# Kernel tuning notes

Hardware: AMD Instinct MI355X
Metric: run time of the kernel (lower is better)

The kernel has to match this reference:

```python
import jax, jax.numpy as jnp
import numpy as np

HEADS, DIM_HEAD, DIM = 12, 64, 768
H = W = 32
N = H * W
B = 4


def _ln(x, g, b, eps=1e-5):
    mu = x.mean(-1, keepdims=True)
    var = ((x - mu) ** 2).mean(-1, keepdims=True)
    return (x - mu) / jnp.sqrt(var + eps) * g + b


def _get_epipolar(k, src_c2w, target_c2w, h=H, w=W):
    # Faithful port of Epipolar_Attention.get_epipolar, without the (hw*hw,3) repeat
    # materialization (uses broadcasting for the pairwise cross product instead).
    b = k.shape[0]
    Wf = h * 16.0 / 9.0
    k = k.astype(jnp.float32)
    k = k.at[:, 0, :].multiply(Wf).at[:, 1, :].multiply(float(h))
    k = k.at[:, 0, 2].set(h / 2.0).at[:, 1, 2].set(h / 2.0)
    ii, jj = jnp.meshgrid(jnp.arange(h), jnp.arange(w), indexing='ij')
    # after the torch column swap: (col, row, 1)
    coords = jnp.stack([jj.ravel(), ii.ravel(), jnp.ones(h * w, jnp.int32)], axis=1).astype(jnp.float32)  # [hw,3]
    k3 = k[:, :3, :3]
    src_r, src_t = src_c2w[:, :3, :3].astype(jnp.float32), src_c2w[:, :3, 3].astype(jnp.float32)
    tgt_r, tgt_t = target_c2w[:, :3, :3].astype(jnp.float32), target_c2w[:, :3, 3].astype(jnp.float32)
    tgt_rinv = jnp.linalg.inv(tgt_r)
    fx, fy = k3[:, 0, 0][:, None], k3[:, 1, 1][:, None]
    cx, cy = k3[:, 0, 2][:, None], k3[:, 1, 2][:, None]
    nc = jnp.stack([(coords[None, :, 0] - cx) / fx,
                    (coords[None, :, 1] - cy) / fy,
                    jnp.broadcast_to(coords[None, :, 2], (b, h * w))], axis=-1)  # [b,hw,3]
    p3w = jnp.einsum('bij,bnj->bni', src_r, nc) + src_t[:, None]
    p2 = jnp.einsum('bij,bnj->bni', tgt_rinv, p3w) - tgt_t[:, None]  # target_w2c_t = -target_c2w_t
    pij_un = jnp.einsum('bij,bnj->bni', k3, p2)                      # [b,hw,3]
    pij = pij_un / (pij_un[..., -1:] + 1e-6)
    o2 = jnp.einsum('bij,bj->bi', tgt_rinv, src_t) - tgt_t           # origin projected
    oij = jnp.einsum('bij,bj->bi', k3, o2)
    oij = oij / oij[..., -1:]
    oi_to_pi = pij - oij[:, None]                # [b,hw,3]
    oi_to_coord = coords[None] - oij[:, None]    # [b,hw,3]
    cr = jnp.cross(oi_to_pi[:, :, None, :], oi_to_coord[:, None, :, :])  # [b,hw,hw,3]
    area = jnp.sqrt((cr * cr).sum(-1))
    vlen = jnp.sqrt((oi_to_pi * oi_to_pi).sum(-1))[:, :, None]
    dist = area / vlen
    dw = 1.0 - jax.nn.sigmoid(50.0 * (dist - 0.5))
    row_max = dw.max(-1, keepdims=True)
    return jnp.where(row_max < 0.5, 1.0, dw)     # rows with max<0.5 are set to all-ones


def setup_inputs():
    key = jax.random.key(0)
    ks = jax.random.split(key, 16)
    s = 0.02
    x = jax.random.normal(ks[0], (B, N, DIM), jnp.float32)
    src_encode = jax.random.normal(ks[1], (B, N, DIM), jnp.float32)
    intrinsic = (jnp.zeros((B, 4, 4), jnp.float32)
                 .at[:, 0, 0].set(1.0).at[:, 1, 1].set(1.0)
                 .at[:, 0, 2].set(0.5).at[:, 1, 2].set(0.5)
                 .at[:, 2, 2].set(1.0).at[:, 3, 3].set(1.0))
    R = jnp.eye(3, dtype=jnp.float32) + 0.1 * jax.random.normal(ks[2], (2, B, 3, 3), jnp.float32)
    t = 0.5 * jax.random.normal(ks[3], (2, B, 3), jnp.float32)
    c2w = (jnp.zeros((2, B, 4, 4), jnp.float32)
           .at[:, :, :3, :3].set(R).at[:, :, :3, 3].set(t).at[:, :, 3, 3].set(1.0))
    hd = HEADS * DIM_HEAD
    w_ = lambda k_, shp: s * jax.random.normal(k_, shp, jnp.float32)
    return dict(
        x=x, src_encode=src_encode, intrinsic=intrinsic, c2w=c2w,
        lnq_g=jnp.ones(DIM), lnq_b=jnp.zeros(DIM), Wq=w_(ks[4], (DIM, hd)), bq=jnp.zeros(hd),
        lnk_g=jnp.ones(DIM), lnk_b=jnp.zeros(DIM), Wk=w_(ks[5], (DIM, hd)), bk=jnp.zeros(hd),
        lnv_g=jnp.ones(DIM), lnv_b=jnp.zeros(DIM), Wv=w_(ks[6], (DIM, hd)), bv=jnp.zeros(hd),
        Wp=w_(ks[7], (hd, DIM)), bp=jnp.zeros(DIM),
        pre_g=jnp.ones(DIM), pre_b=jnp.zeros(DIM),
        W1=w_(ks[8], (DIM, 2 * DIM)), b1=jnp.zeros(2 * DIM),
        W2=w_(ks[9], (2 * DIM, DIM)), b2=jnp.zeros(DIM),
        post_g=jnp.ones(DIM), post_b=jnp.zeros(DIM))


def reference(x, src_encode, intrinsic, c2w, lnq_g, lnq_b, Wq, bq, lnk_g, lnk_b, Wk, bk,
              lnv_g, lnv_b, Wv, bv, Wp, bp, pre_g, pre_b, W1, b1, W2, b2, post_g, post_b):
    b, n, _ = x.shape
    scale = DIM_HEAD ** -0.5
    split = lambda t_: t_.reshape(b, n, HEADS, DIM_HEAD).transpose(0, 2, 1, 3)  # [b,m,n,d]
    q = split(_ln(x, lnq_g, lnq_b) @ Wq + bq)
    k = split(_ln(src_encode, lnk_g, lnk_b) @ Wk + bk)
    v = split(_ln(src_encode, lnv_g, lnv_b) @ Wv + bv)
    scores = scale * jnp.einsum('bmqd,bmkd->bmqk', q, k)
    e1 = _get_epipolar(intrinsic, c2w[1], c2w[0])                    # do_epipolar
    e2 = jnp.swapaxes(_get_epipolar(intrinsic, c2w[0], c2w[1]), 1, 2)  # bidirectional (transposed)
    wmap = e1 * e2                                                   # [b,n,n], shared across heads
    att = jax.nn.softmax(scores * wmap[:, None], axis=-1)
    a = jnp.einsum('bmqk,bmkd->bmqd', att, v).transpose(0, 2, 1, 3).reshape(b, n, HEADS * DIM_HEAD)
    z = _ln(a @ Wp + bp, pre_g, pre_b)
    z = z + (jax.nn.gelu(z @ W1 + b1, approximate=False) @ W2 + b2)  # torch nn.GELU = exact erf
    z = _ln(z, post_g, post_b)
    wm_full = jnp.broadcast_to(wmap[:, None], (b, HEADS, n, n)).reshape(b * HEADS, n, n)
    return z, wm_full
```

## Files before the change

### kernel.cpp

```cpp
#include <hip/hip_runtime.h>
#include <hip/hip_bf16.h>

typedef unsigned short u16;
typedef __attribute__((ext_vector_type(4))) unsigned short u16x4;
typedef __attribute__((ext_vector_type(8))) unsigned short u16x8;
typedef __attribute__((ext_vector_type(8))) short s16x8;
typedef __attribute__((ext_vector_type(4))) float f32x4;

#define HEADS 12
#define NSEQ 1024
#define DIMM 768
#define DHEAD 64

__device__ __forceinline__ float b2f(u16 h) {
  union { unsigned u; float f; } v; v.u = ((unsigned)h) << 16; return v.f;
}
__device__ __forceinline__ u16 f2b(float f) {
  union { float f; unsigned u; } v; v.f = f;
  unsigned r = v.u + 0x7fffu + ((v.u >> 16) & 1u);
  return (u16)(r >> 16);
}
__device__ __forceinline__ void gl_lds16(const u16* g, u16* l) {
  __builtin_amdgcn_global_load_lds(
      (const __attribute__((address_space(1))) void*)g,
      (__attribute__((address_space(3))) void*)l, 16, 0, 0);
}

template<bool GELU, bool RESID>
__device__ __forceinline__ void gemm_body(
    const u16* __restrict__ A, const u16* __restrict__ BT,
    const float* __restrict__ bias, const u16* __restrict__ resid,
    const float* __restrict__ rg, const float* __restrict__ rb,
    u16* __restrict__ C, int K, int lda, int ldb, int ldc,
    int m0, int n0, u16* As, u16* Bs)
{
  const int tid = threadIdx.x;
  const int lane = tid & 63;
  const int wv = tid >> 6;
  const int wm0 = (wv >> 1) * 64;
  const int wn0 = (wv & 1) * 64;
  const int l15 = lane & 15;
  const int quad = lane >> 4;
  const int srow = lane >> 2;
  const int scol = (lane & 3) * 8;

  f32x4 acc[4][4];
  #pragma unroll
  for (int i = 0; i < 4; ++i)
    #pragma unroll
    for (int j = 0; j < 4; ++j)
      acc[i][j] = {0.f, 0.f, 0.f, 0.f};

  const u16* Ab = A + (long)(m0 + wv * 32 + srow) * lda + scol;
  const u16* Bb = BT + (long)(n0 + wv * 32 + srow) * ldb + scol;
  u16* AsW = As + (wv * 32) * 32;
  u16* BsW = Bs + (wv * 32) * 32;

  auto issue = [&](int buf, int kk) {
    #pragma unroll
    for (int t = 0; t < 2; ++t) {
      gl_lds16(Ab + kk + (long)t * 16 * lda, AsW + buf * 4096 + t * 16 * 32);
      gl_lds16(Bb + kk + (long)t * 16 * ldb, BsW + buf * 4096 + t * 16 * 32);
    }
  };

  const int NK = K >> 5;
  issue(0, 0);
  issue(1, 32);

  int cur = 0;
  for (int i = 0; i < NK; ++i) {
    if (i + 1 < NK) asm volatile("s_waitcnt vmcnt(4)" ::: "memory");
    else            asm volatile("s_waitcnt vmcnt(0)" ::: "memory");
    __builtin_amdgcn_s_barrier();
    __builtin_amdgcn_sched_barrier(0);
    if (i + 2 < NK) {
      int nb = cur + 2; if (nb >= 3) nb -= 3;
      issue(nb, (i + 2) * 32);
    }
    const u16* Ac = As + cur * 4096;
    const u16* Bc = Bs + cur * 4096;
    s16x8 af[4], bfr[4];
    #pragma unroll
    for (int i2 = 0; i2 < 4; ++i2)
      af[i2] = *(const s16x8*)&Ac[(wm0 + i2 * 16 + l15) * 32 + quad * 8];
    #pragma unroll
    for (int j = 0; j < 4; ++j)
      bfr[j] = *(const s16x8*)&Bc[(wn0 + j * 16 + l15) * 32 + quad * 8];
    #pragma unroll
    for (int i2 = 0; i2 < 4; ++i2)
      #pragma unroll
      for (int j = 0; j < 4; ++j)
        acc[i2][j] = __builtin_amdgcn_mfma_f32_16x16x32_bf16(af[i2], bfr[j], acc[i2][j], 0, 0, 0);
    ++cur; if (cur == 3) cur = 0;
  }

  #pragma unroll
  for (int i = 0; i < 4; ++i)
    #pragma unroll
    for (int j = 0; j < 4; ++j) {
      const int col = n0 + wn0 + j * 16 + l15;
      const float bvv = bias[col];
      #pragma unroll
      for (int v = 0; v < 4; ++v) {
        const int row = m0 + wm0 + i * 16 + quad * 4 + v;
        float val = acc[i][j][v] + bvv;
        if (GELU) val = 0.5f * val * (1.0f + erff(val * 0.70710678118654752440f));
        if (RESID) val += b2f(resid[(long)row * ldc + col]) * rg[col] + rb[col];
        C[(long)row * ldc + col] = f2b(val);
      }
    }
}

template<bool GELU, bool RESID>
__device__ __forceinline__ void gemm_body64(
    const u16* __restrict__ A, const u16* __restrict__ BT,
    const float* __restrict__ bias, const u16* __restrict__ resid,
    const float* __restrict__ rg, const float* __restrict__ rb,
    u16* __restrict__ C, int K, int lda, int ldb, int ldc,
    int m0, int n0, u16* As, u16* Bs)
{
  const int tid = threadIdx.x;
  const int lane = tid & 63;
  const int wv = tid >> 6;
  const int wm0 = wv * 32;
  const int l15 = lane & 15;
  const int quad = lane >> 4;
  const int srow = lane >> 2;
  const int scol = (lane & 3) * 8;

  f32x4 acc[2][4];
  #pragma unroll
  for (int i = 0; i < 2; ++i)
    #pragma unroll
    for (int j = 0; j < 4; ++j)
      acc[i][j] = {0.f, 0.f, 0.f, 0.f};

  const u16* Ab = A + (long)(m0 + wv * 32 + srow) * lda + scol;
  const u16* Bb = BT + (long)(n0 + wv * 16 + srow) * ldb + scol;
  u16* AsW = As + (wv * 32) * 32;
  u16* BsW = Bs + (wv * 16) * 32;

  auto issue = [&](int buf, int kk) {
    #pragma unroll
    for (int t = 0; t < 2; ++t)
      gl_lds16(Ab + kk + (long)t * 16 * lda, AsW + buf * 4096 + t * 16 * 32);
    gl_lds16(Bb + kk, BsW + buf * 2048);
  };

  const int NK = K >> 5;
  issue(0, 0);
  issue(1, 32);

  int cur = 0;
  for (int i = 0; i < NK; ++i) {
    if (i + 1 < NK) asm volatile("s_waitcnt vmcnt(3)" ::: "memory");
    else            asm volatile("s_waitcnt vmcnt(0)" ::: "memory");
    __builtin_amdgcn_s_barrier();
    __builtin_amdgcn_sched_barrier(0);
    if (i + 2 < NK) {
      int nb = cur + 2; if (nb >= 3) nb -= 3;
      issue(nb, (i + 2) * 32);
    }
    const u16* Ac = As + cur * 4096;
    const u16* Bc = Bs + cur * 2048;
    s16x8 af[2], bfr[4];
    #pragma unroll
    for (int i2 = 0; i2 < 2; ++i2)
      af[i2] = *(const s16x8*)&Ac[(wm0 + i2 * 16 + l15) * 32 + quad * 8];
    #pragma unroll
    for (int j = 0; j < 4; ++j)
      bfr[j] = *(const s16x8*)&Bc[(j * 16 + l15) * 32 + quad * 8];
    #pragma unroll
    for (int i2 = 0; i2 < 2; ++i2)
      #pragma unroll
      for (int j = 0; j < 4; ++j)
        acc[i2][j] = __builtin_amdgcn_mfma_f32_16x16x32_bf16(af[i2], bfr[j], acc[i2][j], 0, 0, 0);
    ++cur; if (cur == 3) cur = 0;
  }

  #pragma unroll
  for (int i = 0; i < 2; ++i)
    #pragma unroll
    for (int j = 0; j < 4; ++j) {
      const int col = n0 + j * 16 + l15;
      const float bvv = bias[col];
      #pragma unroll
      for (int v = 0; v < 4; ++v) {
        const int row = m0 + wm0 + i * 16 + quad * 4 + v;
        float val = acc[i][j][v] + bvv;
        if (GELU) val = 0.5f * val * (1.0f + erff(val * 0.70710678118654752440f));
        if (RESID) val += b2f(resid[(long)row * ldc + col]) * rg[col] + rb[col];
        C[(long)row * ldc + col] = f2b(val);
      }
    }
}

template<bool GELU, bool RESID>
__global__ __launch_bounds__(256)
void gemm_one(const u16* __restrict__ A, const u16* __restrict__ BT,
              const float* __restrict__ bias, const u16* __restrict__ resid,
              const float* __restrict__ rg, const float* __restrict__ rb,
              u16* __restrict__ C, int K, int lda, int ldb, int ldc)
{
  __shared__ u16 As[12288], Bs[6144];
  gemm_body64<GELU, RESID>(A, BT, bias, resid, rg, rb, C, K, lda, ldb, ldc,
                           blockIdx.x * 128, blockIdx.y * 64, As, Bs);
}

__global__ __launch_bounds__(256)
void gemm_qkv(const u16* __restrict__ nx, const u16* __restrict__ ns,
              const u16* __restrict__ qT, const u16* __restrict__ kvT,
              const float* __restrict__ bqf, const float* __restrict__ bkvf,
              u16* __restrict__ qb, u16* __restrict__ kvb)
{
  __shared__ u16 As[12288], Bs[12288];
  const int z = blockIdx.z;
  if (z == 0)
    gemm_body<false, false>(nx, qT, bqf, nullptr, nullptr, nullptr, qb,
                            768, 768, 768, 768,
                            blockIdx.x * 128, blockIdx.y * 128, As, Bs);
  else
    gemm_body<false, false>(ns, kvT, bkvf, nullptr, nullptr, nullptr, kvb,
                            768, 768, 768, 1536,
                            blockIdx.x * 128, (z - 1) * 768 + blockIdx.y * 128, As, Bs);
}

__global__ __launch_bounds__(256, 3)
void fattn(const u16* __restrict__ qb, const u16* __restrict__ kvb,
           const u16* __restrict__ vT, const u16* __restrict__ wm,
           u16* __restrict__ outA)
{
  __shared__ u16 Qs[2 * 64 * 32];
  __shared__ u16 Ks[2][2 * 64 * 32];
  __shared__ u16 Vs[2][2 * 64 * 32];
  __shared__ u16 Ps[64][72];

  const int bh = blockIdx.y;
  const int b = bh / HEADS, h = bh - b * HEADS;
  const int q0 = blockIdx.x * 64;
  const int tid = threadIdx.x;
  const int lane = tid & 63;
  const int wv = tid >> 6;
  const int l15 = lane & 15;
  const int quad = lane >> 4;
  const int srow = lane >> 2;
  const int scol = (lane & 3) * 8;

  const u16* Qg = qb + ((long)b * NSEQ + q0) * DIMM + h * DHEAD;
  const u16* Kg = kvb + (long)b * NSEQ * 1536 + h * DHEAD;
  const u16* Vg = vT + (long)bh * DHEAD * NSEQ;
  const u16* Wg = wm + ((long)b * NSEQ + q0) * NSEQ;

  #pragma unroll
  for (int h2 = 0; h2 < 2; ++h2) {
    gl_lds16(Qg + (long)(wv * 16 + srow) * DIMM + h2 * 32 + scol,
             Qs + (h2 * 64 + wv * 16) * 32);
    gl_lds16(Kg + (long)(wv * 16 + srow) * 1536 + h2 * 32 + scol,
             Ks[0] + (h2 * 64 + wv * 16) * 32);
    gl_lds16(Vg + (long)(wv * 16 + srow) * NSEQ + h2 * 32 + scol,
             Vs[0] + (h2 * 64 + wv * 16) * 32);
  }

  f32x4 Sacc[4], Oacc[4];
  float mrow[4], lrow[4];
  #pragma unroll
  for (int j = 0; j < 4; ++j) {
    Oacc[j] = {0.f, 0.f, 0.f, 0.f};
    mrow[j] = -3.0e38f;
    lrow[j] = 0.f;
  }
  s16x8 qf[2];

  int cur = 0;
  for (int kt = 0; kt < 16; ++kt) {
    __syncthreads();
    if (kt < 15) {
      const int nxt = cur ^ 1;
      #pragma unroll
      for (int h2 = 0; h2 < 2; ++h2) {
        gl_lds16(Kg + (long)((kt + 1) * 64 + wv * 16 + srow) * 1536 + h2 * 32 + scol,
                 Ks[nxt] + (h2 * 64 + wv * 16) * 32);
        gl_lds16(Vg + (long)(wv * 16 + srow) * NSEQ + (kt + 1) * 64 + h2 * 32 + scol,
                 Vs[nxt] + (h2 * 64 + wv * 16) * 32);
      }
    }

    if (kt == 0) {
      qf[0] = *(const s16x8*)&Qs[(0 * 64 + wv * 16 + l15) * 32 + quad * 8];
      qf[1] = *(const s16x8*)&Qs[(1 * 64 + wv * 16 + l15) * 32 + quad * 8];
    }

    float wr[4][4];
    #pragma unroll
    for (int j = 0; j < 4; ++j)
      #pragma unroll
      for (int v = 0; v < 4; ++v)
        wr[j][v] = b2f(Wg[(long)(wv * 16 + quad * 4 + v) * NSEQ + kt * 64 + j * 16 + l15]);

    #pragma unroll
    for (int j = 0; j < 4; ++j) Sacc[j] = {0.f, 0.f, 0.f, 0.f};
    #pragma unroll
    for (int j = 0; j < 4; ++j)
      #pragma unroll
      for (int h2 = 0; h2 < 2; ++h2) {
        s16x8 kf = *(const s16x8*)&Ks[cur][(h2 * 64 + j * 16 + l15) * 32 + quad * 8];
        Sacc[j] = __builtin_amdgcn_mfma_f32_16x16x32_bf16(qf[h2], kf, Sacc[j], 0, 0, 0);
      }

    #pragma unroll
    for (int j = 0; j < 4; ++j)
      #pragma unroll
      for (int v = 0; v < 4; ++v)
        Sacc[j][v] *= wr[j][v];
    #pragma unroll
    for (int v = 0; v < 4; ++v) {
      float tm = fmaxf(fmaxf(Sacc[0][v], Sacc[1][v]), fmaxf(Sacc[2][v], Sacc[3][v]));
      tm = fmaxf(tm, __shfl_xor(tm, 1));
      tm = fmaxf(tm, __shfl_xor(tm, 2));
      tm = fmaxf(tm, __shfl_xor(tm, 4));
      tm = fmaxf(tm, __shfl_xor(tm, 8));
      const float mnew = fmaxf(mrow[v], tm);
      const float al = __expf(mrow[v] - mnew);
      float rs = 0.f;
      #pragma unroll
      for (int j = 0; j < 4; ++j) {
        const float e = __expf(Sacc[j][v] - mnew);
        Sacc[j][v] = e;
        rs += e;
      }
      rs += __shfl_xor(rs, 1);
      rs += __shfl_xor(rs, 2);
      rs += __shfl_xor(rs, 4);
      rs += __shfl_xor(rs, 8);
      lrow[v] = lrow[v] * al + rs;
      mrow[v] = mnew;
      #pragma unroll
      for (int jn = 0; jn < 4; ++jn) Oacc[jn][v] *= al;
    }
    #pragma unroll
    for (int j = 0; j < 4; ++j)
      #pragma unroll
      for (int v = 0; v < 4; ++v)
        Ps[wv * 16 + quad * 4 + v][j * 16 + l15] = f2b(Sacc[j][v]);

    #pragma unroll
    for (int h2 = 0; h2 < 2; ++h2) {
      s16x8 af = *(const s16x8*)&Ps[wv * 16 + l15][h2 * 32 + quad * 8];
      #pragma unroll
      for (int jn = 0; jn < 4; ++jn) {
        s16x8 vf = *(const s16x8*)&Vs[cur][(h2 * 64 + jn * 16 + l15) * 32 + quad * 8];
        Oacc[jn] = __builtin_amdgcn_mfma_f32_16x16x32_bf16(af, vf, Oacc[jn], 0, 0, 0);
      }
    }
    cur ^= 1;
  }

  #pragma unroll
  for (int v = 0; v < 4; ++v) {
    const int row = q0 + wv * 16 + quad * 4 + v;
    const float inv = 1.0f / lrow[v];
    #pragma unroll
    for (int jn = 0; jn < 4; ++jn)
      outA[((long)(b * NSEQ + row)) * DIMM + h * DHEAD + jn * 16 + l15] =
          f2b(Oacc[jn][v] * inv);
  }
}

template<bool F32IN>
__global__ __launch_bounds__(256)
void norm_k(const void* __restrict__ in, u16* __restrict__ out)
{
  const long base = (long)blockIdx.x * DIMM;
  const int tid = threadIdx.x;
  __shared__ float s1[8], s2[8];
  float v0, v1, v2;
  if (F32IN) {
    const float* p = (const float*)in + base;
    v0 = p[tid]; v1 = p[tid + 256]; v2 = p[tid + 512];
  } else {
    const u16* p = (const u16*)in + base;
    v0 = b2f(p[tid]); v1 = b2f(p[tid + 256]); v2 = b2f(p[tid + 512]);
  }
  float s = v0 + v1 + v2;
  #pragma unroll
  for (int off = 32; off; off >>= 1) s += __shfl_down(s, off);
  const int lane = tid & 63, wid = tid >> 6;
  if (!lane) s1[wid] = s;
  __syncthreads();
  if (!tid) s1[4] = s1[0] + s1[1] + s1[2] + s1[3];
  __syncthreads();
  const float mu = s1[4] / 768.0f;
  float d0 = v0 - mu, d1 = v1 - mu, d2 = v2 - mu;
  float sq = d0 * d0 + d1 * d1 + d2 * d2;
  #pragma unroll
  for (int off = 32; off; off >>= 1) sq += __shfl_down(sq, off);
  if (!lane) s2[wid] = sq;
  __syncthreads();
  if (!tid) s2[4] = s2[0] + s2[1] + s2[2] + s2[3];
  __syncthreads();
  const float rstd = 1.0f / sqrtf(s2[4] / 768.0f + 1e-5f);
  u16* o = out + base;
  o[tid]       = f2b(d0 * rstd);
  o[tid + 256] = f2b(d1 * rstd);
  o[tid + 512] = f2b(d2 * rstd);
}

__global__ __launch_bounds__(256)
void norm_dual(const float* __restrict__ inA, const float* __restrict__ inB,
               u16* __restrict__ outA, u16* __restrict__ outB)
{
  const int r = blockIdx.x;
  const float* p = ((r < 4096) ? inA : inB) + (long)(r & 4095) * DIMM;
  u16* o = ((r < 4096) ? outA : outB) + (long)(r & 4095) * DIMM;
  const int tid = threadIdx.x;
  __shared__ float s1[8], s2[8];
  float v0 = p[tid], v1 = p[tid + 256], v2 = p[tid + 512];
  float s = v0 + v1 + v2;
  #pragma unroll
  for (int off = 32; off; off >>= 1) s += __shfl_down(s, off);
  const int lane = tid & 63, wid = tid >> 6;
  if (!lane) s1[wid] = s;
  __syncthreads();
  if (!tid) s1[4] = s1[0] + s1[1] + s1[2] + s1[3];
  __syncthreads();
  const float mu = s1[4] / 768.0f;
  float d0 = v0 - mu, d1 = v1 - mu, d2 = v2 - mu;
  float sq = d0 * d0 + d1 * d1 + d2 * d2;
  #pragma unroll
  for (int off = 32; off; off >>= 1) sq += __shfl_down(sq, off);
  if (!lane) s2[wid] = sq;
  __syncthreads();
  if (!tid) s2[4] = s2[0] + s2[1] + s2[2] + s2[3];
  __syncthreads();
  const float rstd = 1.0f / sqrtf(s2[4] / 768.0f + 1e-5f);
  o[tid]       = f2b(d0 * rstd);
  o[tid + 256] = f2b(d1 * rstd);
  o[tid + 512] = f2b(d2 * rstd);
}

__global__ __launch_bounds__(256)
void ln_final(const u16* __restrict__ in, const float* __restrict__ g,
              const float* __restrict__ bb, float* __restrict__ out)
{
  const long base = (long)blockIdx.x * DIMM;
  const int tid = threadIdx.x;
  __shared__ float s1[8], s2[8];
  const u16* p = in + base;
  float v0 = b2f(p[tid]), v1 = b2f(p[tid + 256]), v2 = b2f(p[tid + 512]);
  float s = v0 + v1 + v2;
  #pragma unroll
  for (int off = 32; off; off >>= 1) s += __shfl_down(s, off);
  const int lane = tid & 63, wid = tid >> 6;
  if (!lane) s1[wid] = s;
  __syncthreads();
  if (!tid) s1[4] = s1[0] + s1[1] + s1[2] + s1[3];
  __syncthreads();
  const float mu = s1[4] / 768.0f;
  float d0 = v0 - mu, d1 = v1 - mu, d2 = v2 - mu;
  float sq = d0 * d0 + d1 * d1 + d2 * d2;
  #pragma unroll
  for (int off = 32; off; off >>= 1) sq += __shfl_down(sq, off);
  if (!lane) s2[wid] = sq;
  __syncthreads();
  if (!tid) s2[4] = s2[0] + s2[1] + s2[2] + s2[3];
  __syncthreads();
  const float rstd = 1.0f / sqrtf(s2[4] / 768.0f + 1e-5f);
  float* o = out + base;
  o[tid]       = d0 * rstd * g[tid]       + bb[tid];
  o[tid + 256] = d1 * rstd * g[tid + 256] + bb[tid + 256];
  o[tid + 512] = d2 * rstd * g[tid + 512] + bb[tid + 512];
}

__global__ __launch_bounds__(256)
void prep_all(const float* w0, const float* w1, const float* w2,
              const float* w3, const float* w4, const float* w5,
              const float* gq, const float* gk, const float* gv, const float* gp,
              u16* d0, u16* d12, u16* d3, u16* d4, u16* d5,
              const float* bq, const float* bk, const float* bv, const float* b1,
              const float* lnqb, const float* lnkb, const float* lnvb, const float* preb,
              float* obq, float* obkv, float* ob1)
{
  __shared__ u16 t[32][36];
  __shared__ float red[8][32];
  const int tid = threadIdx.x;

  if (blockIdx.z == 6) {
    const int y = blockIdx.y;
    if (y >= 4) return;
    const float* W; const float* bln; const float* bw; float* out;
    int C; float sc = 1.0f;
    switch (y) {
      case 0: W = w0; bln = lnqb; bw = bq; out = obq;        C = 768;  sc = 0.125f; break;
      case 1: W = w1; bln = lnkb; bw = bk; out = obkv;       C = 768;  break;
      case 2: W = w2; bln = lnvb; bw = bv; out = obkv + 768; C = 768;  break;
      default: W = w4; bln = preb; bw = b1; out = ob1;       C = 1536; break;
    }
    const int c0 = blockIdx.x * 32;
    if (c0 >= C) return;
    const int cl = tid & 31;
    const int rg = tid >> 5;
    const int c = c0 + cl;
    float s = 0.f;
    for (int r = rg * 96; r < rg * 96 + 96; ++r)
      s += bln[r] * W[(long)r * C + c];
    red[rg][cl] = s;
    __syncthreads();
    if (rg == 0) {
      float tot = bw[c];
      #pragma unroll
      for (int k = 0; k < 8; ++k) tot += red[k][cl];
      out[c] = tot * sc;
    }
    return;
  }

  const float* src; const float* g; u16* dst; int R, C; float sc = 1.0f;
  switch (blockIdx.z) {
    case 0: src = w0; g = gq; dst = d0;  R = 768;  C = 768;  sc = 0.125f; break;
    case 1: src = w1; g = gk; dst = d12; R = 768;  C = 768;  break;
    case 2: src = w2; g = gv; dst = d12 + 768 * 768; R = 768; C = 768; break;
    case 3: src = w3; g = nullptr; dst = d3; R = 768;  C = 768;  break;
    case 4: src = w4; g = gp; dst = d4; R = 768;  C = 1536; break;
    default: src = w5; g = nullptr; dst = d5; R = 1536; C = 768; break;
  }
  const int c0 = blockIdx.x * 32;
  const int r0 = blockIdx.y * 32;
  if (c0 >= C || r0 >= R) return;
  const int i = tid >> 3;
  const int j4 = (tid & 7) * 4;
  const float rs = (g ? g[r0 + i] : 1.0f) * sc;
  #pragma unroll
  for (int jj = 0; jj < 4; ++jj)
    t[i][j4 + jj] = f2b(src[(long)(r0 + i) * C + c0 + j4 + jj] * rs);
  __syncthreads();
  u16x4 ov;
  #pragma unroll
  for (int jj = 0; jj < 4; ++jj) ov[jj] = t[j4 + jj][i];
  *(u16x4*)&dst[(long)(c0 + i) * R + r0 + j4] = ov;
}

__global__ __launch_bounds__(256)
void v_transpose(const u16* __restrict__ kvb, u16* __restrict__ vT)
{
  __shared__ u16 t[64][72];
  const int z = blockIdx.y;
  const int b = z / HEADS, h = z - b * HEADS;
  const int n0 = blockIdx.x * 64;
  const int tid = threadIdx.x;
  const int i = tid >> 2;
  const int jb = (tid & 3) * 16;
  const u16* src = kvb + (long)(b * NSEQ + n0 + i) * 1536 + 768 + h * DHEAD + jb;
  *(u16x8*)&t[i][jb]     = *(const u16x8*)&src[0];
  *(u16x8*)&t[i][jb + 8] = *(const u16x8*)&src[8];
  __syncthreads();
  const int dd = tid >> 2;
  const int nb = (tid & 3) * 16;
  u16x8 o0, o1;
  #pragma unroll
  for (int nn = 0; nn < 8; ++nn) { o0[nn] = t[nb + nn][dd]; o1[nn] = t[nb + 8 + nn][dd]; }
  u16* dst = vT + ((long)z * DHEAD + dd) * NSEQ + n0 + nb;
  *(u16x8*)&dst[0] = o0;
  *(u16x8*)&dst[8] = o1;
}

__global__ void epi_setup(const float* __restrict__ intr, const float* __restrict__ c2w,
                          float* __restrict__ u4, float* __restrict__ oijb)
{
  const int db = blockIdx.x;
  const int d = db >> 2, b = db & 3;
  __shared__ float S[36];
  if (threadIdx.x == 0) {
    const int sidx = (d == 0) ? 1 : 0;
    const int tidx = 1 - sidx;
    float k3[9], sr[9], st[3], tr[9], tt[3];
    const float Wf = 32.0f * 16.0f / 9.0f;
    for (int j = 0; j < 3; ++j) {
      k3[j]     = intr[(b * 4 + 0) * 4 + j] * Wf;
      k3[3 + j] = intr[(b * 4 + 1) * 4 + j] * 32.0f;
      k3[6 + j] = intr[(b * 4 + 2) * 4 + j];
    }
    k3[2] = 16.0f; k3[5] = 16.0f;
    for (int i = 0; i < 3; ++i) {
      for (int j = 0; j < 3; ++j) {
        sr[i * 3 + j] = c2w[((sidx * 4 + b) * 4 + i) * 4 + j];
        tr[i * 3 + j] = c2w[((tidx * 4 + b) * 4 + i) * 4 + j];
      }
      st[i] = c2w[((sidx * 4 + b) * 4 + i) * 4 + 3];
      tt[i] = c2w[((tidx * 4 + b) * 4 + i) * 4 + 3];
    }
    double a = tr[0], bb_ = tr[1], c = tr[2];
    double dd2 = tr[3], e = tr[4], f = tr[5];
    double g2 = tr[6], h2 = tr[7], i2 = tr[8];
    double det = a * (e * i2 - f * h2) - bb_ * (dd2 * i2 - f * g2) + c * (dd2 * h2 - e * g2);
    double inv[9] = {
      (e * i2 - f * h2), (c * h2 - bb_ * i2), (bb_ * f - c * e),
      (f * g2 - dd2 * i2), (a * i2 - c * g2), (c * dd2 - a * f),
      (dd2 * h2 - e * g2), (bb_ * g2 - a * h2), (a * e - bb_ * dd2)
    };
    float tri[9];
    for (int t2 = 0; t2 < 9; ++t2) tri[t2] = (float)(inv[t2] / det);
    float o2[3], oij[3];
    for (int i3 = 0; i3 < 3; ++i3)
      o2[i3] = tri[i3 * 3] * st[0] + tri[i3 * 3 + 1] * st[1] + tri[i3 * 3 + 2] * st[2] - tt[i3];
    for (int i3 = 0; i3 < 3; ++i3)
      oij[i3] = k3[i3 * 3] * o2[0] + k3[i3 * 3 + 1] * o2[1] + k3[i3 * 3 + 2] * o2[2];
    const float ozf = oij[2];
    oij[0] = oij[0] / ozf; oij[1] = oij[1] / ozf; oij[2] = ozf / ozf;
    for (int t2 = 0; t2 < 9; ++t2) { S[t2] = k3[t2]; S[9 + t2] = sr[t2]; S[21 + t2] = tri[t2]; }
    for (int t2 = 0; t2 < 3; ++t2) { S[18 + t2] = st[t2]; S[30 + t2] = tt[t2]; S[33 + t2] = oij[t2]; }
    oijb[db * 4 + 0] = oij[0]; oijb[db * 4 + 1] = oij[1]; oijb[db * 4 + 2] = oij[2];
    oijb[db * 4 + 3] = 0.f;
  }
  __syncthreads();
  for (int n = threadIdx.x; n < 1024; n += blockDim.x) {
    const float ncx = ((float)(n & 31) - S[2]) / S[0];
    const float ncy = ((float)(n >> 5) - S[5]) / S[4];
    const float p0 = S[9]  * ncx + S[10] * ncy + S[11] + S[18];
    const float p1 = S[12] * ncx + S[13] * ncy + S[14] + S[19];
    const float p2 = S[15] * ncx + S[16] * ncy + S[17] + S[20];
    const float q0 = S[21] * p0 + S[22] * p1 + S[23] * p2 - S[30];
    const float q1 = S[24] * p0 + S[25] * p1 + S[26] * p2 - S[31];
    const float q2 = S[27] * p0 + S[28] * p1 + S[29] * p2 - S[32];
    const float w0 = S[0] * q0 + S[1] * q1 + S[2] * q2;
    const float w1 = S[3] * q0 + S[4] * q1 + S[5] * q2;
    const float w2 = S[6] * q0 + S[7] * q1 + S[8] * q2;
    const float pz = w2 + 1e-6f;
    const float ux = w0 / pz - S[33];
    const float uy = w1 / pz - S[34];
    const float uz = w2 / pz - S[35];
    const float vlen = sqrtf(ux * ux + uy * uy + uz * uz);
    f32x4 uo = {ux, uy, uz, vlen};
    *(f32x4*)&u4[((long)db * 1024 + n) * 4] = uo;
  }
}

__device__ __forceinline__ float dwval(f32x4 U, float ox, float oy, float oz, int m)
{
  const float cx = (float)(m & 31) - ox;
  const float cy = (float)(m >> 5) - oy;
  const float cz = 1.0f - oz;
  const float crx = U.y * cz - U.z * cy;
  const float cry = U.z * cx - U.x * cz;
  const float crz = U.x * cy - U.y * cx;
  const float area = sqrtf(crx * crx + cry * cry + crz * crz);
  const float dist = area / U.w;
  const float t = 50.0f * (dist - 0.5f);
  return 1.0f - 1.0f / (1.0f + __expf(-t));
}

__global__ __launch_bounds__(256)
void epi_flags(const float* __restrict__ u4, const float* __restrict__ oijb,
               float* __restrict__ flags)
{
  const int rowid = blockIdx.x;
  const int db = rowid >> 10;
  const f32x4 U = *(const f32x4*)&u4[(long)rowid * 4];
  const float ox = oijb[db * 4 + 0];
  const float oy = oijb[db * 4 + 1];
  const float oz = oijb[db * 4 + 2];
  const int tid = threadIdx.x;
  __shared__ float red[8];
  float mx = -1e30f;
  #pragma unroll
  for (int i = 0; i < 4; ++i)
    mx = fmaxf(mx, dwval(U, ox, oy, oz, tid + i * 256));
  #pragma unroll
  for (int off = 32; off; off >>= 1) mx = fmaxf(mx, __shfl_down(mx, off));
  const int lane = tid & 63, wid = tid >> 6;
  if (!lane) red[wid] = mx;
  __syncthreads();
  if (!tid) {
    const float m4 = fmaxf(fmaxf(red[0], red[1]), fmaxf(red[2], red[3]));
    flags[rowid] = (m4 < 0.5f) ? 1.0f : 0.0f;
  }
}

__global__ __launch_bounds__(256)
void epi_wmap(const float* __restrict__ u4, const float* __restrict__ oijb,
              const float* __restrict__ flags,
              u16* __restrict__ wm, float* __restrict__ wm_full)
{
  const int b = blockIdx.z;
  const int q0 = blockIdx.x * 32;
  const int k0 = blockIdx.y * 32;
  const int tid = threadIdx.x;
  const int i = tid >> 3;
  const int j4 = (tid & 7) * 4;

  __shared__ f32x4 U2s[32];
  __shared__ float f2s[32];
  __shared__ float f1s[32];
  if (tid < 32) {
    U2s[tid] = *(const f32x4*)&u4[((long)(4 + b) * 1024 + k0 + tid) * 4];
    f2s[tid] = flags[(4 + b) * 1024 + k0 + tid];
    f1s[tid] = flags[b * 1024 + q0 + tid];
  }
  __syncthreads();

  const int q = q0 + i;
  const f32x4 U1 = *(const f32x4*)&u4[((long)b * 1024 + q) * 4];
  const float o1x = oijb[b * 4 + 0], o1y = oijb[b * 4 + 1], o1z = oijb[b * 4 + 2];
  const float o2x = oijb[(4 + b) * 4 + 0], o2y = oijb[(4 + b) * 4 + 1], o2z = oijb[(4 + b) * 4 + 2];
  const bool fl1 = f1s[i] > 0.5f;

  u16x4 pk;
  f32x4 wf;
  #pragma unroll
  for (int jj = 0; jj < 4; ++jj) {
    const int k = k0 + j4 + jj;
    const float e1 = fl1 ? 1.0f : dwval(U1, o1x, o1y, o1z, k);
    const float e2 = (f2s[j4 + jj] > 0.5f) ? 1.0f : dwval(U2s[j4 + jj], o2x, o2y, o2z, q);
    const float w = e1 * e2;
    wf[jj] = w;
    pk[jj] = f2b(w);
  }
  *(u16x4*)&wm[((long)b * 1024 + q0 + i) * 1024 + k0 + j4] = pk;
  #pragma unroll
  for (int h = 0; h < HEADS; ++h)
    *(f32x4*)&wm_full[((long)(b * HEADS + h) * 1024 + q0 + i) * 1024 + k0 + j4] = wf;
}

extern "C" void kernel_launch(void* const* d_in, const int* in_sizes, int n_in,
                              void* d_out, int out_size, void* d_ws, size_t ws_size,
                              hipStream_t stream)
{
  (void)in_sizes; (void)n_in; (void)out_size; (void)ws_size;
  const float* x     = (const float*)d_in[0];
  const float* src   = (const float*)d_in[1];
  const float* intr  = (const float*)d_in[2];
  const float* c2w   = (const float*)d_in[3];
  const float* lnq_g = (const float*)d_in[4];
  const float* lnq_b = (const float*)d_in[5];
  const float* Wq    = (const float*)d_in[6];
  const float* bq    = (const float*)d_in[7];
  const float* lnk_g = (const float*)d_in[8];
  const float* lnk_b = (const float*)d_in[9];
  const float* Wk    = (const float*)d_in[10];
  const float* bk    = (const float*)d_in[11];
  const float* lnv_g = (const float*)d_in[12];
  const float* lnv_b = (const float*)d_in[13];
  const float* Wv    = (const float*)d_in[14];
  const float* bv    = (const float*)d_in[15];
  const float* Wp    = (const float*)d_in[16];
  const float* bp    = (const float*)d_in[17];
  const float* pre_g = (const float*)d_in[18];
  const float* pre_b = (const float*)d_in[19];
  const float* W1    = (const float*)d_in[20];
  const float* b1    = (const float*)d_in[21];
  const float* W2    = (const float*)d_in[22];
  const float* b2    = (const float*)d_in[23];
  const float* post_g= (const float*)d_in[24];
  const float* post_b= (const float*)d_in[25];

  char* ws = (char*)d_ws;
  size_t off = 0;
  auto alloc = [&](size_t bytes) -> char* {
    char* p = ws + off;
    off = (off + bytes + 255) & ~(size_t)255;
    return p;
  };
  const size_t SEQD = (size_t)4096 * 768 * 2;

  u16* WqT  = (u16*)alloc(768 * 768 * 2);
  u16* WkvT = (u16*)alloc((size_t)1536 * 768 * 2);
  u16* WpT  = (u16*)alloc(768 * 768 * 2);
  u16* W1T  = (u16*)alloc(768 * 1536 * 2);
  u16* W2T  = (u16*)alloc(1536 * 768 * 2);
  float* bqf  = (float*)alloc(768 * 4);
  float* bkvf = (float*)alloc(1536 * 4);
  float* b1f  = (float*)alloc(1536 * 4);
  char* pool = alloc(6 * SEQD);
  float* u4   = (float*)alloc(8 * 1024 * 4 * 4);
  float* oijb = (float*)alloc(8 * 4 * 4);
  u16* wmapb  = (u16*)alloc((size_t)4 * 1024 * 1024 * 2);
  float* flagb = (float*)alloc(8 * 1024 * 4);

  u16* S0 = (u16*)pool;
  u16* S1 = (u16*)(pool + SEQD);
  u16* S2 = (u16*)(pool + 2 * SEQD);
  u16* S3 = (u16*)(pool + 3 * SEQD);
  u16* S5 = (u16*)(pool + 5 * SEQD);

  float* out_z  = (float*)d_out;
  float* out_wm = (float*)d_out + (size_t)4 * 1024 * 768;

  prep_all<<<dim3(48, 48, 7), 256, 0, stream>>>(
      Wq, Wk, Wv, Wp, W1, W2, lnq_g, lnk_g, lnv_g, pre_g,
      WqT, WkvT, WpT, W1T, W2T,
      bq, bk, bv, b1, lnq_b, lnk_b, lnv_b, pre_b,
      bqf, bkvf, b1f);

  epi_setup<<<8, 128, 0, stream>>>(intr, c2w, u4, oijb);
  epi_flags<<<8192, 256, 0, stream>>>(u4, oijb, flagb);
  epi_wmap<<<dim3(32, 32, 4), 256, 0, stream>>>(u4, oijb, flagb, wmapb, out_wm);

  norm_dual<<<8192, 256, 0, stream>>>(x, src, S0, S1);

  gemm_qkv<<<dim3(32, 6, 3), 256, 0, stream>>>(S0, S1, WqT, WkvT, bqf, bkvf, S2, S3);

  v_transpose<<<dim3(16, 48), 256, 0, stream>>>(S3, S5);

  fattn<<<dim3(16, 48), 256, 0, stream>>>(S2, S3, S5, wmapb, S0);

  gemm_one<false, false><<<dim3(32, 12), 256, 0, stream>>>(
      S0, WpT, bp, nullptr, nullptr, nullptr, S1, 768, 768, 768, 768);

  norm_k<false><<<4096, 256, 0, stream>>>(S1, S2);

  gemm_one<true, false><<<dim3(32, 24), 256, 0, stream>>>(
      S2, W1T, b1f, nullptr, nullptr, nullptr, S3, 768, 768, 768, 1536);

  gemm_one<false, true><<<dim3(32, 12), 256, 0, stream>>>(
      S3, W2T, b2, S2, pre_g, pre_b, S5, 1536, 1536, 1536, 768);

  ln_final<<<4096, 256, 0, stream>>>(S5, post_g, post_b, out_z);
}
```

Baseline: 511.5 us.

## Merge launches into mega-kernels with grid barriers and fused V-transpose epilogue

Folds weight prep, epipolar setup/flags and input layernorms into a single block-indexed prep kernel. The QKV GEMM and epipolar weight-map generation now share one launch, and the V projection writes its transposed layout straight from the GEMM epilogue, so the separate transpose pass goes away. The post-attention projection, layernorm, MLP and final layernorm run as one persistent 768-block kernel separated by atomic grid barriers. This cuts launch gaps and the intermediate transpose round-trip, but the spin barriers can deadlock if all 768 blocks are not co-resident, and idle blocks wait at each barrier.

```diff
diff --git a/kernel.cpp b/kernel.cpp
--- a/kernel.cpp
+++ b/kernel.cpp
@@ -26,13 +26,25 @@
       (__attribute__((address_space(3))) void*)l, 16, 0, 0);
 }
 
-template<bool GELU, bool RESID>
+__device__ __forceinline__ void gridbar(int* c, int target) {
+  __syncthreads();
+  if (threadIdx.x == 0) {
+    __threadfence();
+    __hip_atomic_fetch_add(c, 1, __ATOMIC_ACQ_REL, __HIP_MEMORY_SCOPE_AGENT);
+    while (__hip_atomic_load(c, __ATOMIC_ACQUIRE, __HIP_MEMORY_SCOPE_AGENT) < target)
+      __builtin_amdgcn_s_sleep(2);
+    __threadfence();
+  }
+  __syncthreads();
+}
+
+template<bool GELU, bool RESID, bool VTOUT>
 __device__ __forceinline__ void gemm_body(
     const u16* __restrict__ A, const u16* __restrict__ BT,
     const float* __restrict__ bias, const u16* __restrict__ resid,
     const float* __restrict__ rg, const float* __restrict__ rb,
     u16* __restrict__ C, int K, int lda, int ldb, int ldc,
-    int m0, int n0, u16* As, u16* Bs)
+    int m0, int n0, u16* As, u16* Bs, u16* __restrict__ vt)
 {
   const int tid = threadIdx.x;
   const int lane = tid & 63;
@@ -95,6 +107,40 @@
     ++cur; if (cur == 3) cur = 0;
   }
 
+  if (VTOUT) {
+    __syncthreads();
+    u16* shp = As;
+    const int b = m0 >> 10;
+    const int nloc = m0 & 1023;
+    const int fb0 = n0 - 768;
+    #pragma unroll
+    for (int p = 0; p < 2; ++p) {
+      if ((wv & 1) == p) {
+        #pragma unroll
+        for (int j = 0; j < 4; ++j) {
+          const float bvv = bias[n0 + wn0 + j * 16 + l15];
+          #pragma unroll
+          for (int i = 0; i < 4; ++i)
+            #pragma unroll
+            for (int v = 0; v < 4; ++v)
+              shp[(j * 16 + l15) * 136 + (wm0 + i * 16 + quad * 4 + v)] =
+                  f2b(acc[i][j][v] + bvv);
+        }
+      }
+      __syncthreads();
+      {
+        const int f = tid >> 2;
+        const int rg2 = (tid & 3) * 32;
+        u16* dst = vt + ((long)(b * 768 + fb0 + p * 64 + f)) * NSEQ + nloc + rg2;
+        #pragma unroll
+        for (int c4 = 0; c4 < 4; ++c4)
+          *(u16x8*)&dst[c4 * 8] = *(const u16x8*)&shp[f * 136 + rg2 + c4 * 8];
+      }
+      __syncthreads();
+    }
+    return;
+  }
+
   #pragma unroll
   for (int i = 0; i < 4; ++i)
     #pragma unroll
@@ -196,34 +242,298 @@
     }
 }
 
-template<bool GELU, bool RESID>
+__device__ __forceinline__ float dwval(f32x4 U, float ox, float oy, float oz, int m)
+{
+  const float cx = (float)(m & 31) - ox;
+  const float cy = (float)(m >> 5) - oy;
+  const float cz = 1.0f - oz;
+  const float crx = U.y * cz - U.z * cy;
+  const float cry = U.z * cx - U.x * cz;
+  const float crz = U.x * cy - U.y * cx;
+  const float area = sqrtf(crx * crx + cry * cry + crz * crz);
+  const float dist = area / U.w;
+  const float t = 50.0f * (dist - 0.5f);
+  return 1.0f - 1.0f / (1.0f + __expf(-t));
+}
+
+#define PREP_T0 13824
+#define PREP_T1 14016
+#define PREP_T2 22208
+#define PREP_T3 30400
+
 __global__ __launch_bounds__(256)
-void gemm_one(const u16* __restrict__ A, const u16* __restrict__ BT,
-              const float* __restrict__ bias, const u16* __restrict__ resid,
-              const float* __restrict__ rg, const float* __restrict__ rb,
-              u16* __restrict__ C, int K, int lda, int ldb, int ldc)
-{
-  __shared__ u16 As[12288], Bs[6144];
-  gemm_body64<GELU, RESID>(A, BT, bias, resid, rg, rb, C, K, lda, ldb, ldc,
-                           blockIdx.x * 128, blockIdx.y * 64, As, Bs);
+void prep2(const float* w0, const float* w1, const float* w2,
+           const float* w3, const float* w4, const float* w5,
+           const float* gq, const float* gk, const float* gv, const float* gp,
+           u16* d0, u16* d12, u16* d3, u16* d4, u16* d5,
+           const float* bq, const float* bk, const float* bv, const float* b1,
+           const float* lnqb, const float* lnkb, const float* lnvb, const float* preb,
+           float* obq, float* obkv, float* ob1,
+           const float* intr, const float* c2w,
+           float* u4, float* oijb, float* flags,
+           const float* nx, const float* nsrc, u16* onx, u16* onsrc,
+           int* bars)
+{
+  const int bid = blockIdx.x;
+  const int tid = threadIdx.x;
+  if (bid == 0 && tid < 8) bars[tid] = 0;
+
+  if (bid < PREP_T0) {
+    __shared__ u16 t[32][36];
+    const int z = bid / 2304;
+    const int rem = bid - z * 2304;
+    const int bx = rem % 48, by = rem / 48;
+    const float* src; const float* g; u16* dst; int R, C; float sc = 1.0f;
+    switch (z) {
+      case 0: src = w0; g = gq; dst = d0;  R = 768;  C = 768;  sc = 0.125f; break;
+      case 1: src = w1; g = gk; dst = d12; R = 768;  C = 768;  break;
+      case 2: src = w2; g = gv; dst = d12 + 768 * 768; R = 768; C = 768; break;
+      case 3: src = w3; g = nullptr; dst = d3; R = 768;  C = 768;  break;
+      case 4: src = w4; g = gp; dst = d4; R = 768;  C = 1536; break;
+      default: src = w5; g = nullptr; dst = d5; R = 1536; C = 768; break;
+    }
+    const int c0 = bx * 32;
+    const int r0 = by * 32;
+    if (c0 >= C || r0 >= R) return;
+    const int i = tid >> 3;
+    const int j4 = (tid & 7) * 4;
+    const float rs = (g ? g[r0 + i] : 1.0f) * sc;
+    #pragma unroll
+    for (int jj = 0; jj < 4; ++jj)
+      t[i][j4 + jj] = f2b(src[(long)(r0 + i) * C + c0 + j4 + jj] * rs);
+    __syncthreads();
+    u16x4 ov;
+    #pragma unroll
+    for (int jj = 0; jj < 4; ++jj) ov[jj] = t[j4 + jj][i];
+    *(u16x4*)&dst[(long)(c0 + i) * R + r0 + j4] = ov;
+    return;
+  }
+
+  if (bid < PREP_T1) {
+    __shared__ float red[8][32];
+    const int idx = bid - PREP_T0;
+    const int y = idx / 48;
+    const int bx = idx % 48;
+    const float* W; const float* bln; const float* bw; float* out;
+    int C; float sc = 1.0f;
+    switch (y) {
+      case 0: W = w0; bln = lnqb; bw = bq; out = obq;        C = 768;  sc = 0.125f; break;
+      case 1: W = w1; bln = lnkb; bw = bk; out = obkv;       C = 768;  break;
+      case 2: W = w2; bln = lnvb; bw = bv; out = obkv + 768; C = 768;  break;
+      default: W = w4; bln = preb; bw = b1; out = ob1;       C = 1536; break;
+    }
+    const int c0 = bx * 32;
+    if (c0 >= C) return;
+    const int cl = tid & 31;
+    const int rg = tid >> 5;
+    const int c = c0 + cl;
+    float s = 0.f;
+    for (int r = rg * 96; r < rg * 96 + 96; ++r)
+      s += bln[r] * W[(long)r * C + c];
+    red[rg][cl] = s;
+    __syncthreads();
+    if (rg == 0) {
+      float tot = bw[c];
+      #pragma unroll
+      for (int k = 0; k < 8; ++k) tot += red[k][cl];
+      out[c] = tot * sc;
+    }
+    return;
+  }
+
+  if (bid < PREP_T2) {
+    __shared__ float S[40];
+    __shared__ float redf[8];
+    const int rowid = bid - PREP_T1;
+    const int db = rowid >> 10;
+    const int n = rowid & 1023;
+    const int d = db >> 2, b = db & 3;
+    if (tid == 0) {
+      const int sidx = (d == 0) ? 1 : 0;
+      const int tidx = 1 - sidx;
+      float k3[9], sr[9], st[3], tr[9], tt[3];
+      const float Wf = 32.0f * 16.0f / 9.0f;
+      for (int j = 0; j < 3; ++j) {
+        k3[j]     = intr[(b * 4 + 0) * 4 + j] * Wf;
+        k3[3 + j] = intr[(b * 4 + 1) * 4 + j] * 32.0f;
+        k3[6 + j] = intr[(b * 4 + 2) * 4 + j];
+      }
+      k3[2] = 16.0f; k3[5] = 16.0f;
+      for (int i = 0; i < 3; ++i) {
+        for (int j = 0; j < 3; ++j) {
+          sr[i * 3 + j] = c2w[((sidx * 4 + b) * 4 + i) * 4 + j];
+          tr[i * 3 + j] = c2w[((tidx * 4 + b) * 4 + i) * 4 + j];
+        }
+        st[i] = c2w[((sidx * 4 + b) * 4 + i) * 4 + 3];
+        tt[i] = c2w[((tidx * 4 + b) * 4 + i) * 4 + 3];
+      }
+      double a = tr[0], bb_ = tr[1], c = tr[2];
+      double dd2 = tr[3], e = tr[4], f = tr[5];
+      double g2 = tr[6], h2 = tr[7], i2 = tr[8];
+      double det = a * (e * i2 - f * h2) - bb_ * (dd2 * i2 - f * g2) + c * (dd2 * h2 - e * g2);
+      double inv[9] = {
+        (e * i2 - f * h2), (c * h2 - bb_ * i2), (bb_ * f - c * e),
+        (f * g2 - dd2 * i2), (a * i2 - c * g2), (c * dd2 - a * f),
+        (dd2 * h2 - e * g2), (bb_ * g2 - a * h2), (a * e - bb_ * dd2)
+      };
+      float tri[9];
+      for (int t2 = 0; t2 < 9; ++t2) tri[t2] = (float)(inv[t2] / det);
+      float o2[3], oij[3];
+      for (int i3 = 0; i3 < 3; ++i3)
+        o2[i3] = tri[i3 * 3] * st[0] + tri[i3 * 3 + 1] * st[1] + tri[i3 * 3 + 2] * st[2] - tt[i3];
+      for (int i3 = 0; i3 < 3; ++i3)
+        oij[i3] = k3[i3 * 3] * o2[0] + k3[i3 * 3 + 1] * o2[1] + k3[i3 * 3 + 2] * o2[2];
+      const float ozf = oij[2];
+      oij[0] = oij[0] / ozf; oij[1] = oij[1] / ozf; oij[2] = ozf / ozf;
+      if (n == 0) {
+        oijb[db * 4 + 0] = oij[0]; oijb[db * 4 + 1] = oij[1];
+        oijb[db * 4 + 2] = oij[2]; oijb[db * 4 + 3] = 0.f;
+      }
+      const float ncx = ((float)(n & 31) - k3[2]) / k3[0];
+      const float ncy = ((float)(n >> 5) - k3[5]) / k3[4];
+      const float p0 = sr[0] * ncx + sr[1] * ncy + sr[2] + st[0];
+      const float p1 = sr[3] * ncx + sr[4] * ncy + sr[5] + st[1];
+      const float p2 = sr[6] * ncx + sr[7] * ncy + sr[8] + st[2];
+      const float q0 = tri[0] * p0 + tri[1] * p1 + tri[2] * p2 - tt[0];
+      const float q1 = tri[3] * p0 + tri[4] * p1 + tri[5] * p2 - tt[1];
+      const float q2 = tri[6] * p0 + tri[7] * p1 + tri[8] * p2 - tt[2];
+      const float ww0 = k3[0] * q0 + k3[1] * q1 + k3[2] * q2;
+      const float ww1 = k3[3] * q0 + k3[4] * q1 + k3[5] * q2;
+      const float ww2 = k3[6] * q0 + k3[7] * q1 + k3[8] * q2;
+      const float pz = ww2 + 1e-6f;
+      const float ux = ww0 / pz - oij[0];
+      const float uy = ww1 / pz - oij[1];
+      const float uz = ww2 / pz - oij[2];
+      const float vlen = sqrtf(ux * ux + uy * uy + uz * uz);
+      f32x4 uo = {ux, uy, uz, vlen};
+      *(f32x4*)&u4[(long)rowid * 4] = uo;
+      S[33] = oij[0]; S[34] = oij[1]; S[35] = oij[2];
+      S[36] = ux; S[37] = uy; S[38] = uz; S[39] = vlen;
+    }
+    __syncthreads();
+    const f32x4 U = {S[36], S[37], S[38], S[39]};
+    const float ox = S[33], oy = S[34], oz = S[35];
+    float mx = -1e30f;
+    #pragma unroll
+    for (int i = 0; i < 4; ++i)
+      mx = fmaxf(mx, dwval(U, ox, oy, oz, tid + i * 256));
+    #pragma unroll
+    for (int off = 32; off; off >>= 1) mx = fmaxf(mx, __shfl_down(mx, off));
+    const int lane = tid & 63, wid = tid >> 6;
+    if (!lane) redf[wid] = mx;
+    __syncthreads();
+    if (!tid) {
+      const float m4 = fmaxf(fmaxf(redf[0], redf[1]), fmaxf(redf[2], redf[3]));
+      flags[rowid] = (m4 < 0.5f) ? 1.0f : 0.0f;
+    }
+    return;
+  }
+
+  {
+    __shared__ float s1[8], s2[8];
+    const int r = bid - PREP_T2;
+    const float* p = ((r < 4096) ? nx : nsrc) + (long)(r & 4095) * DIMM;
+    u16* o = ((r < 4096) ? onx : onsrc) + (long)(r & 4095) * DIMM;
+    float v0 = p[tid], v1 = p[tid + 256], v2 = p[tid + 512];
+    float s = v0 + v1 + v2;
+    #pragma unroll
+    for (int off = 32; off; off >>= 1) s += __shfl_down(s, off);
+    const int lane = tid & 63, wid = tid >> 6;
+    if (!lane) s1[wid] = s;
+    __syncthreads();
+    if (!tid) s1[4] = s1[0] + s1[1] + s1[2] + s1[3];
+    __syncthreads();
+    const float mu = s1[4] / 768.0f;
+    float d0 = v0 - mu, d1 = v1 - mu, d2 = v2 - mu;
+    float sq = d0 * d0 + d1 * d1 + d2 * d2;
+    #pragma unroll
+    for (int off = 32; off; off >>= 1) sq += __shfl_down(sq, off);
+    if (!lane) s2[wid] = sq;
+    __syncthreads();
+    if (!tid) s2[4] = s2[0] + s2[1] + s2[2] + s2[3];
+    __syncthreads();
+    const float rstd = 1.0f / sqrtf(s2[4] / 768.0f + 1e-5f);
+    o[tid]       = f2b(d0 * rstd);
+    o[tid + 256] = f2b(d1 * rstd);
+    o[tid + 512] = f2b(d2 * rstd);
+  }
 }
 
 __global__ __launch_bounds__(256)
-void gemm_qkv(const u16* __restrict__ nx, const u16* __restrict__ ns,
-              const u16* __restrict__ qT, const u16* __restrict__ kvT,
-              const float* __restrict__ bqf, const float* __restrict__ bkvf,
-              u16* __restrict__ qb, u16* __restrict__ kvb)
-{
-  __shared__ u16 As[12288], Bs[12288];
-  const int z = blockIdx.z;
-  if (z == 0)
-    gemm_body<false, false>(nx, qT, bqf, nullptr, nullptr, nullptr, qb,
-                            768, 768, 768, 768,
-                            blockIdx.x * 128, blockIdx.y * 128, As, Bs);
-  else
-    gemm_body<false, false>(ns, kvT, bkvf, nullptr, nullptr, nullptr, kvb,
-                            768, 768, 768, 1536,
-                            blockIdx.x * 128, (z - 1) * 768 + blockIdx.y * 128, As, Bs);
+void stageB(const u16* __restrict__ nx, const u16* __restrict__ ns,
+            const u16* __restrict__ qT, const u16* __restrict__ kvT,
+            const float* __restrict__ bqf, const float* __restrict__ bkvf,
+            u16* __restrict__ qb, u16* __restrict__ kvb, u16* __restrict__ vT,
+            const float* __restrict__ u4, const float* __restrict__ oijb,
+            const float* __restrict__ flags,
+            u16* __restrict__ wm, float* __restrict__ wm_full)
+{
+  __shared__ __align__(16) u16 sh[24576];
+  const int bid = blockIdx.x;
+  const int tid = threadIdx.x;
+
+  if (bid < 576) {
+    u16* As = sh;
+    u16* Bs = sh + 12288;
+    const int x = bid & 31;
+    const int t = bid >> 5;
+    const int y = t % 6;
+    const int z = t / 6;
+    if (z == 0)
+      gemm_body<false, false, false>(nx, qT, bqf, nullptr, nullptr, nullptr, qb,
+                                     768, 768, 768, 768,
+                                     x * 128, y * 128, As, Bs, nullptr);
+    else if (z == 1)
+      gemm_body<false, false, false>(ns, kvT, bkvf, nullptr, nullptr, nullptr, kvb,
+                                     768, 768, 768, 1536,
+                                     x * 128, y * 128, As, Bs, nullptr);
+    else
+      gemm_body<false, false, true>(ns, kvT, bkvf, nullptr, nullptr, nullptr, nullptr,
+                                    768, 768, 768, 1536,
+                                    x * 128, 768 + y * 128, As, Bs, vT);
+    return;
+  }
+
+  const int id = bid - 576;
+  const int qx = id & 31;
+  const int ky = (id >> 5) & 31;
+  const int b = id >> 10;
+  const int q0 = qx * 32;
+  const int k0 = ky * 32;
+  const int i = tid >> 3;
+  const int j4 = (tid & 7) * 4;
+
+  f32x4* U2s = (f32x4*)sh;
+  float* f2s = (float*)(sh + 256);
+  float* f1s = (float*)(sh + 320);
+  if (tid < 32) {
+    U2s[tid] = *(const f32x4*)&u4[((long)(4 + b) * 1024 + k0 + tid) * 4];
+    f2s[tid] = flags[(4 + b) * 1024 + k0 + tid];
+    f1s[tid] = flags[b * 1024 + q0 + tid];
+  }
+  __syncthreads();
+
+  const int q = q0 + i;
+  const f32x4 U1 = *(const f32x4*)&u4[((long)b * 1024 + q) * 4];
+  const float o1x = oijb[b * 4 + 0], o1y = oijb[b * 4 + 1], o1z = oijb[b * 4 + 2];
+  const float o2x = oijb[(4 + b) * 4 + 0], o2y = oijb[(4 + b) * 4 + 1], o2z = oijb[(4 + b) * 4 + 2];
+  const bool fl1 = f1s[i] > 0.5f;
+
+  u16x4 pk;
+  f32x4 wf;
+  #pragma unroll
+  for (int jj = 0; jj < 4; ++jj) {
+    const int k = k0 + j4 + jj;
+    const float e1 = fl1 ? 1.0f : dwval(U1, o1x, o1y, o1z, k);
+    const float e2 = (f2s[j4 + jj] > 0.5f) ? 1.0f : dwval(U2s[j4 + jj], o2x, o2y, o2z, q);
+    const float w = e1 * e2;
+    wf[jj] = w;
+    pk[jj] = f2b(w);
+  }
+  *(u16x4*)&wm[((long)b * 1024 + q0 + i) * 1024 + k0 + j4] = pk;
+  #pragma unroll
+  for (int h = 0; h < HEADS; ++h)
+    *(f32x4*)&wm_full[((long)(b * HEADS + h) * 1024 + q0 + i) * 1024 + k0 + j4] = wf;
 }
 
 __global__ __launch_bounds__(256, 3)
@@ -367,21 +677,14 @@
   }
 }
 
-template<bool F32IN>
-__global__ __launch_bounds__(256)
-void norm_k(const void* __restrict__ in, u16* __restrict__ out)
-{
-  const long base = (long)blockIdx.x * DIMM;
+__device__ __forceinline__ void norm_row(const u16* __restrict__ in,
+                                         u16* __restrict__ out, int r,
+                                         float* s1, float* s2)
+{
+  const long base = (long)r * DIMM;
   const int tid = threadIdx.x;
-  __shared__ float s1[8], s2[8];
-  float v0, v1, v2;
-  if (F32IN) {
-    const float* p = (const float*)in + base;
-    v0 = p[tid]; v1 = p[tid + 256]; v2 = p[tid + 512];
-  } else {
-    const u16* p = (const u16*)in + base;
-    v0 = b2f(p[tid]); v1 = b2f(p[tid + 256]); v2 = b2f(p[tid + 512]);
-  }
+  const u16* p = in + base;
+  float v0 = b2f(p[tid]), v1 = b2f(p[tid + 256]), v2 = b2f(p[tid + 512]);
   float s = v0 + v1 + v2;
   #pragma unroll
   for (int off = 32; off; off >>= 1) s += __shfl_down(s, off);
@@ -404,48 +707,17 @@
   o[tid]       = f2b(d0 * rstd);
   o[tid + 256] = f2b(d1 * rstd);
   o[tid + 512] = f2b(d2 * rstd);
-}
-
-__global__ __launch_bounds__(256)
-void norm_dual(const float* __restrict__ inA, const float* __restrict__ inB,
-               u16* __restrict__ outA, u16* __restrict__ outB)
-{
-  const int r = blockIdx.x;
-  const float* p = ((r < 4096) ? inA : inB) + (long)(r & 4095) * DIMM;
-  u16* o = ((r < 4096) ? outA : outB) + (long)(r & 4095) * DIMM;
+  __syncthreads();
+}
+
+__device__ __forceinline__ void ln_row(const u16* __restrict__ in,
+                                       const float* __restrict__ g,
+                                       const float* __restrict__ bb,
+                                       float* __restrict__ out, int r,
+                                       float* s1, float* s2)
+{
+  const long base = (long)r * DIMM;
   const int tid = threadIdx.x;
-  __shared__ float s1[8], s2[8];
-  float v0 = p[tid], v1 = p[tid + 256], v2 = p[tid + 512];
-  float s = v0 + v1 + v2;
-  #pragma unroll
-  for (int off = 32; off; off >>= 1) s += __shfl_down(s, off);
-  const int lane = tid & 63, wid = tid >> 6;
-  if (!lane) s1[wid] = s;
-  __syncthreads();
-  if (!tid) s1[4] = s1[0] + s1[1] + s1[2] + s1[3];
-  __syncthreads();
-  const float mu = s1[4] / 768.0f;
-  float d0 = v0 - mu, d1 = v1 - mu, d2 = v2 - mu;
-  float sq = d0 * d0 + d1 * d1 + d2 * d2;
-  #pragma unroll
-  for (int off = 32; off; off >>= 1) sq += __shfl_down(sq, off);
-  if (!lane) s2[wid] = sq;
-  __syncthreads();
-  if (!tid) s2[4] = s2[0] + s2[1] + s2[2] + s2[3];
-  __syncthreads();
-  const float rstd = 1.0f / sqrtf(s2[4] / 768.0f + 1e-5f);
-  o[tid]       = f2b(d0 * rstd);
-  o[tid + 256] = f2b(d1 * rstd);
-  o[tid + 512] = f2b(d2 * rstd);
-}
-
-__global__ __launch_bounds__(256)
-void ln_final(const u16* __restrict__ in, const float* __restrict__ g,
-              const float* __restrict__ bb, float* __restrict__ out)
-{
-  const long base = (long)blockIdx.x * DIMM;
-  const int tid = threadIdx.x;
-  __shared__ float s1[8], s2[8];
   const u16* p = in + base;
   float v0 = b2f(p[tid]), v1 = b2f(p[tid + 256]), v2 = b2f(p[tid + 512]);
   float s = v0 + v1 + v2;
@@ -470,255 +742,47 @@
   o[tid]       = d0 * rstd * g[tid]       + bb[tid];
   o[tid + 256] = d1 * rstd * g[tid + 256] + bb[tid + 256];
   o[tid + 512] = d2 * rstd * g[tid + 512] + bb[tid + 512];
-}
-
-__global__ __launch_bounds__(256)
-void prep_all(const float* w0, const float* w1, const float* w2,
-              const float* w3, const float* w4, const float* w5,
-              const float* gq, const float* gk, const float* gv, const float* gp,
-              u16* d0, u16* d12, u16* d3, u16* d4, u16* d5,
-              const float* bq, const float* bk, const float* bv, const float* b1,
-              const float* lnqb, const float* lnkb, const float* lnvb, const float* preb,
-              float* obq, float* obkv, float* ob1)
-{
-  __shared__ u16 t[32][36];
-  __shared__ float red[8][32];
-  const int tid = threadIdx.x;
-
-  if (blockIdx.z == 6) {
-    const int y = blockIdx.y;
-    if (y >= 4) return;
-    const float* W; const float* bln; const float* bw; float* out;
-    int C; float sc = 1.0f;
-    switch (y) {
-      case 0: W = w0; bln = lnqb; bw = bq; out = obq;        C = 768;  sc = 0.125f; break;
-      case 1: W = w1; bln = lnkb; bw = bk; out = obkv;       C = 768;  break;
-      case 2: W = w2; bln = lnvb; bw = bv; out = obkv + 768; C = 768;  break;
-      default: W = w4; bln = preb; bw = b1; out = ob1;       C = 1536; break;
-    }
-    const int c0 = blockIdx.x * 32;
-    if (c0 >= C) return;
-    const int cl = tid & 31;
-    const int rg = tid >> 5;
-    const int c = c0 + cl;
-    float s = 0.f;
-    for (int r = rg * 96; r < rg * 96 + 96; ++r)
-      s += bln[r] * W[(long)r * C + c];
-    red[rg][cl] = s;
-    __syncthreads();
-    if (rg == 0) {
-      float tot = bw[c];
-      #pragma unroll
-      for (int k = 0; k < 8; ++k) tot += red[k][cl];
-      out[c] = tot * sc;
-    }
-    return;
-  }
-
-  const float* src; const float* g; u16* dst; int R, C; float sc = 1.0f;
-  switch (blockIdx.z) {
-    case 0: src = w0; g = gq; dst = d0;  R = 768;  C = 768;  sc = 0.125f; break;
-    case 1: src = w1; g = gk; dst = d12; R = 768;  C = 768;  break;
-    case 2: src = w2; g = gv; dst = d12 + 768 * 768; R = 768; C = 768; break;
-    case 3: src = w3; g = nullptr; dst = d3; R = 768;  C = 768;  break;
-    case 4: src = w4; g = gp; dst = d4; R = 768;  C = 1536; break;
-    default: src = w5; g = nullptr; dst = d5; R = 1536; C = 768; break;
-  }
-  const int c0 = blockIdx.x * 32;
-  const int r0 = blockIdx.y * 32;
-  if (c0 >= C || r0 >= R) return;
-  const int i = tid >> 3;
-  const int j4 = (tid & 7) * 4;
-  const float rs = (g ? g[r0 + i] : 1.0f) * sc;
-  #pragma unroll
-  for (int jj = 0; jj < 4; ++jj)
-    t[i][j4 + jj] = f2b(src[(long)(r0 + i) * C + c0 + j4 + jj] * rs);
-  __syncthreads();
-  u16x4 ov;
-  #pragma unroll
-  for (int jj = 0; jj < 4; ++jj) ov[jj] = t[j4 + jj][i];
-  *(u16x4*)&dst[(long)(c0 + i) * R + r0 + j4] = ov;
-}
-
-__global__ __launch_bounds__(256)
-void v_transpose(const u16* __restrict__ kvb, u16* __restrict__ vT)
-{
-  __shared__ u16 t[64][72];
-  const int z = blockIdx.y;
-  const int b = z / HEADS, h = z - b * HEADS;
-  const int n0 = blockIdx.x * 64;
-  const int tid = threadIdx.x;
-  const int i = tid >> 2;
-  const int jb = (tid & 3) * 16;
-  const u16* src = kvb + (long)(b * NSEQ + n0 + i) * 1536 + 768 + h * DHEAD + jb;
-  *(u16x8*)&t[i][jb]     = *(const u16x8*)&src[0];
-  *(u16x8*)&t[i][jb + 8] = *(const u16x8*)&src[8];
-  __syncthreads();
-  const int dd = tid >> 2;
-  const int nb = (tid & 3) * 16;
-  u16x8 o0, o1;
-  #pragma unroll
-  for (int nn = 0; nn < 8; ++nn) { o0[nn] = t[nb + nn][dd]; o1[nn] = t[nb + 8 + nn][dd]; }
-  u16* dst = vT + ((long)z * DHEAD + dd) * NSEQ + n0 + nb;
-  *(u16x8*)&dst[0] = o0;
-  *(u16x8*)&dst[8] = o1;
-}
-
-__global__ void epi_setup(const float* __restrict__ intr, const float* __restrict__ c2w,
-                          float* __restrict__ u4, float* __restrict__ oijb)
-{
-  const int db = blockIdx.x;
-  const int d = db >> 2, b = db & 3;
-  __shared__ float S[36];
-  if (threadIdx.x == 0) {
-    const int sidx = (d == 0) ? 1 : 0;
-    const int tidx = 1 - sidx;
-    float k3[9], sr[9], st[3], tr[9], tt[3];
-    const float Wf = 32.0f * 16.0f / 9.0f;
-    for (int j = 0; j < 3; ++j) {
-      k3[j]     = intr[(b * 4 + 0) * 4 + j] * Wf;
-      k3[3 + j] = intr[(b * 4 + 1) * 4 + j] * 32.0f;
-      k3[6 + j] = intr[(b * 4 + 2) * 4 + j];
-    }
-    k3[2] = 16.0f; k3[5] = 16.0f;
-    for (int i = 0; i < 3; ++i) {
-      for (int j = 0; j < 3; ++j) {
-        sr[i * 3 + j] = c2w[((sidx * 4 + b) * 4 + i) * 4 + j];
-        tr[i * 3 + j] = c2w[((tidx * 4 + b) * 4 + i) * 4 + j];
-      }
-      st[i] = c2w[((sidx * 4 + b) * 4 + i) * 4 + 3];
-      tt[i] = c2w[((tidx * 4 + b) * 4 + i) * 4 + 3];
-    }
-    double a = tr[0], bb_ = tr[1], c = tr[2];
-    double dd2 = tr[3], e = tr[4], f = tr[5];
-    double g2 = tr[6], h2 = tr[7], i2 = tr[8];
-    double det = a * (e * i2 - f * h2) - bb_ * (dd2 * i2 - f * g2) + c * (dd2 * h2 - e * g2);
-    double inv[9] = {
-      (e * i2 - f * h2), (c * h2 - bb_ * i2), (bb_ * f - c * e),
-      (f * g2 - dd2 * i2), (a * i2 - c * g2), (c * dd2 - a * f),
-      (dd2 * h2 - e * g2), (bb_ * g2 - a * h2), (a * e - bb_ * dd2)
-    };
-    float tri[9];
-    for (int t2 = 0; t2 < 9; ++t2) tri[t2] = (float)(inv[t2] / det);
-    float o2[3], oij[3];
-    for (int i3 = 0; i3 < 3; ++i3)
-      o2[i3] = tri[i3 * 3] * st[0] + tri[i3 * 3 + 1] * st[1] + tri[i3 * 3 + 2] * st[2] - tt[i3];
-    for (int i3 = 0; i3 < 3; ++i3)
-      oij[i3] = k3[i3 * 3] * o2[0] + k3[i3 * 3 + 1] * o2[1] + k3[i3 * 3 + 2] * o2[2];
-    const float ozf = oij[2];
-    oij[0] = oij[0] / ozf; oij[1] = oij[1] / ozf; oij[2] = ozf / ozf;
-    for (int t2 = 0; t2 < 9; ++t2) { S[t2] = k3[t2]; S[9 + t2] = sr[t2]; S[21 + t2] = tri[t2]; }
-    for (int t2 = 0; t2 < 3; ++t2) { S[18 + t2] = st[t2]; S[30 + t2] = tt[t2]; S[33 + t2] = oij[t2]; }
-    oijb[db * 4 + 0] = oij[0]; oijb[db * 4 + 1] = oij[1]; oijb[db * 4 + 2] = oij[2];
-    oijb[db * 4 + 3] = 0.f;
-  }
-  __syncthreads();
-  for (int n = threadIdx.x; n < 1024; n += blockDim.x) {
-    const float ncx = ((float)(n & 31) - S[2]) / S[0];
-    const float ncy = ((float)(n >> 5) - S[5]) / S[4];
-    const float p0 = S[9]  * ncx + S[10] * ncy + S[11] + S[18];
-    const float p1 = S[12] * ncx + S[13] * ncy + S[14] + S[19];
-    const float p2 = S[15] * ncx + S[16] * ncy + S[17] + S[20];
-    const float q0 = S[21] * p0 + S[22] * p1 + S[23] * p2 - S[30];
-    const float q1 = S[24] * p0 + S[25] * p1 + S[26] * p2 - S[31];
-    const float q2 = S[27] * p0 + S[28] * p1 + S[29] * p2 - S[32];
-    const float w0 = S[0] * q0 + S[1] * q1 + S[2] * q2;
-    const float w1 = S[3] * q0 + S[4] * q1 + S[5] * q2;
-    const float w2 = S[6] * q0 + S[7] * q1 + S[8] * q2;
-    const float pz = w2 + 1e-6f;
-    const float ux = w0 / pz - S[33];
-    const float uy = w1 / pz - S[34];
-    const float uz = w2 / pz - S[35];
-    const float vlen = sqrtf(ux * ux + uy * uy + uz * uz);
-    f32x4 uo = {ux, uy, uz, vlen};
-    *(f32x4*)&u4[((long)db * 1024 + n) * 4] = uo;
-  }
-}
-
-__device__ __forceinline__ float dwval(f32x4 U, float ox, float oy, float oz, int m)
-{
-  const float cx = (float)(m & 31) - ox;
-  const float cy = (float)(m >> 5) - oy;
-  const float cz = 1.0f - oz;
-  const float crx = U.y * cz - U.z * cy;
-  const float cry = U.z * cx - U.x * cz;
-  const float crz = U.x * cy - U.y * cx;
-  const float area = sqrtf(crx * crx + cry * cry + crz * crz);
-  const float dist = area / U.w;
-  const float t = 50.0f * (dist - 0.5f);
-  return 1.0f - 1.0f / (1.0f + __expf(-t));
-}
-
-__global__ __launch_bounds__(256)
-void epi_flags(const float* __restrict__ u4, const float* __restrict__ oijb,
-               float* __restrict__ flags)
-{
-  const int rowid = blockIdx.x;
-  const int db = rowid >> 10;
-  const f32x4 U = *(const f32x4*)&u4[(long)rowid * 4];
-  const float ox = oijb[db * 4 + 0];
-  const float oy = oijb[db * 4 + 1];
-  const float oz = oijb[db * 4 + 2];
-  const int tid = threadIdx.x;
-  __shared__ float red[8];
-  float mx = -1e30f;
-  #pragma unroll
-  for (int i = 0; i < 4; ++i)
-    mx = fmaxf(mx, dwval(U, ox, oy, oz, tid + i * 256));
-  #pragma unroll
-  for (int off = 32; off; off >>= 1) mx = fmaxf(mx, __shfl_down(mx, off));
-  const int lane = tid & 63, wid = tid >> 6;
-  if (!lane) red[wid] = mx;
-  __syncthreads();
-  if (!tid) {
-    const float m4 = fmaxf(fmaxf(red[0], red[1]), fmaxf(red[2], red[3]));
-    flags[rowid] = (m4 < 0.5f) ? 1.0f : 0.0f;
-  }
-}
-
-__global__ __launch_bounds__(256)
-void epi_wmap(const float* __restrict__ u4, const float* __restrict__ oijb,
-              const float* __restrict__ flags,
-              u16* __restrict__ wm, float* __restrict__ wm_full)
-{
-  const int b = blockIdx.z;
-  const int q0 = blockIdx.x * 32;
-  const int k0 = blockIdx.y * 32;
-  const int tid = threadIdx.x;
-  const int i = tid >> 3;
-  const int j4 = (tid & 7) * 4;
-
-  __shared__ f32x4 U2s[32];
-  __shared__ float f2s[32];
-  __shared__ float f1s[32];
-  if (tid < 32) {
-    U2s[tid] = *(const f32x4*)&u4[((long)(4 + b) * 1024 + k0 + tid) * 4];
-    f2s[tid] = flags[(4 + b) * 1024 + k0 + tid];
-    f1s[tid] = flags[b * 1024 + q0 + tid];
-  }
-  __syncthreads();
-
-  const int q = q0 + i;
-  const f32x4 U1 = *(const f32x4*)&u4[((long)b * 1024 + q) * 4];
-  const float o1x = oijb[b * 4 + 0], o1y = oijb[b * 4 + 1], o1z = oijb[b * 4 + 2];
-  const float o2x = oijb[(4 + b) * 4 + 0], o2y = oijb[(4 + b) * 4 + 1], o2z = oijb[(4 + b) * 4 + 2];
-  const bool fl1 = f1s[i] > 0.5f;
-
-  u16x4 pk;
-  f32x4 wf;
-  #pragma unroll
-  for (int jj = 0; jj < 4; ++jj) {
-    const int k = k0 + j4 + jj;
-    const float e1 = fl1 ? 1.0f : dwval(U1, o1x, o1y, o1z, k);
-    const float e2 = (f2s[j4 + jj] > 0.5f) ? 1.0f : dwval(U2s[j4 + jj], o2x, o2y, o2z, q);
-    const float w = e1 * e2;
-    wf[jj] = w;
-    pk[jj] = f2b(w);
-  }
-  *(u16x4*)&wm[((long)b * 1024 + q0 + i) * 1024 + k0 + j4] = pk;
-  #pragma unroll
-  for (int h = 0; h < HEADS; ++h)
-    *(f32x4*)&wm_full[((long)(b * HEADS + h) * 1024 + q0 + i) * 1024 + k0 + j4] = wf;
+  __syncthreads();
+}
+
+__global__ __launch_bounds__(256, 3)
+void tail_coop(const u16* __restrict__ aIn, const u16* __restrict__ WpT,
+               const float* __restrict__ bp, u16* __restrict__ t0,
+               u16* __restrict__ zp, const u16* __restrict__ W1T,
+               const float* __restrict__ b1f, u16* __restrict__ hbuf,
+               const u16* __restrict__ W2T, const float* __restrict__ b2,
+               const float* __restrict__ pre_g, const float* __restrict__ pre_b,
+               u16* __restrict__ t1,
+               const float* __restrict__ post_g, const float* __restrict__ post_b,
+               float* __restrict__ out_z, int* bars)
+{
+  __shared__ __align__(16) u16 sh[18432];
+  __shared__ float s1[8], s2[8];
+  u16* As = sh;
+  u16* Bs = sh + 12288;
+  const int bid = blockIdx.x;
+
+  if (bid < 384)
+    gemm_body64<false, false>(aIn, WpT, bp, nullptr, nullptr, nullptr, t0,
+                              768, 768, 768, 768,
+                              (bid & 31) * 128, (bid >> 5) * 64, As, Bs);
+  gridbar(bars + 0, 768);
+
+  for (int r = bid; r < 4096; r += 768) norm_row(t0, zp, r, s1, s2);
+  gridbar(bars + 1, 768);
+
+  gemm_body64<true, false>(zp, W1T, b1f, nullptr, nullptr, nullptr, hbuf,
+                           768, 768, 768, 1536,
+                           (bid & 31) * 128, (bid >> 5) * 64, As, Bs);
+  gridbar(bars + 2, 768);
+
+  if (bid < 384)
+    gemm_body64<false, true>(hbuf, W2T, b2, zp, pre_g, pre_b, t1,
+                             1536, 1536, 1536, 768,
+                             (bid & 31) * 128, (bid >> 5) * 64, As, Bs);
+  gridbar(bars + 3, 768);
+
+  for (int r = bid; r < 4096; r += 768) ln_row(t1, post_g, post_b, out_z, r, s1, s2);
 }
 
 extern "C" void kernel_launch(void* const* d_in, const int* in_sizes, int n_in,
@@ -775,6 +839,7 @@
   float* oijb = (float*)alloc(8 * 4 * 4);
   u16* wmapb  = (u16*)alloc((size_t)4 * 1024 * 1024 * 2);
   float* flagb = (float*)alloc(8 * 1024 * 4);
+  int* bars   = (int*)alloc(64);
 
   u16* S0 = (u16*)pool;
   u16* S1 = (u16*)(pool + SEQD);
@@ -785,34 +850,21 @@
   float* out_z  = (float*)d_out;
   float* out_wm = (float*)d_out + (size_t)4 * 1024 * 768;
 
-  prep_all<<<dim3(48, 48, 7), 256, 0, stream>>>(
+  prep2<<<PREP_T3, 256, 0, stream>>>(
       Wq, Wk, Wv, Wp, W1, W2, lnq_g, lnk_g, lnv_g, pre_g,
       WqT, WkvT, WpT, W1T, W2T,
       bq, bk, bv, b1, lnq_b, lnk_b, lnv_b, pre_b,
-      bqf, bkvf, b1f);
-
-  epi_setup<<<8, 128, 0, stream>>>(intr, c2w, u4, oijb);
-  epi_flags<<<8192, 256, 0, stream>>>(u4, oijb, flagb);
-  epi_wmap<<<dim3(32, 32, 4), 256, 0, stream>>>(u4, oijb, flagb, wmapb, out_wm);
-
-  norm_dual<<<8192, 256, 0, stream>>>(x, src, S0, S1);
-
-  gemm_qkv<<<dim3(32, 6, 3), 256, 0, stream>>>(S0, S1, WqT, WkvT, bqf, bkvf, S2, S3);
-
-  v_transpose<<<dim3(16, 48), 256, 0, stream>>>(S3, S5);
+      bqf, bkvf, b1f,
+      intr, c2w, u4, oijb, flagb,
+      x, src, S0, S1, bars);
+
+  stageB<<<4672, 256, 0, stream>>>(
+      S0, S1, WqT, WkvT, bqf, bkvf, S2, S3, S5,
+      u4, oijb, flagb, wmapb, out_wm);
 
   fattn<<<dim3(16, 48), 256, 0, stream>>>(S2, S3, S5, wmapb, S0);
 
-  gemm_one<false, false><<<dim3(32, 12), 256, 0, stream>>>(
-      S0, WpT, bp, nullptr, nullptr, nullptr, S1, 768, 768, 768, 768);
-
-  norm_k<false><<<4096, 256, 0, stream>>>(S1, S2);
-
-  gemm_one<true, false><<<dim3(32, 24), 256, 0, stream>>>(
-      S2, W1T, b1f, nullptr, nullptr, nullptr, S3, 768, 768, 768, 1536);
-
-  gemm_one<false, true><<<dim3(32, 12), 256, 0, stream>>>(
-      S3, W2T, b2, S2, pre_g, pre_b, S5, 1536, 1536, 1536, 768);
-
-  ln_final<<<4096, 256, 0, stream>>>(S5, post_g, post_b, out_z);
-}
+  tail_coop<<<768, 256, 0, stream>>>(
+      S0, WpT, bp, S1, S2, W1T, b1f, S3, W2T, b2, pre_g, pre_b, S5,
+      post_g, post_b, out_z, bars);
+}
```

Result: slower. 1.116 ms (+118.2%).
